# Kernel optimization log

Hardware: AMD Instinct MI355X
Metric: run time of the kernel (lower is better)

## Reference

```python
import jax, jax.numpy as jnp
import numpy as np

B, S, D = 4, 2048, 1024
H = 16
HD = D // H  # 64


def _xavier(key, shape):
    fan_in, fan_out = shape[1], shape[0]
    limit = float(np.sqrt(6.0 / (fan_in + fan_out)))
    return jax.random.uniform(key, shape, jnp.float32, -limit, limit)


def setup_inputs() -> dict:
    key = jax.random.key(0)
    ks = jax.random.split(key, 5)
    x = jax.random.normal(ks[0], (B, S, D), dtype=jnp.float32)
    # nn.Linear weights are [out, in]; biases zero-initialized
    Wq = _xavier(ks[1], (D, D)); bq = jnp.zeros((D,), jnp.float32)
    Wk = _xavier(ks[2], (D, D)); bk = jnp.zeros((D,), jnp.float32)
    Wv = _xavier(ks[3], (D, D)); bv = jnp.zeros((D,), jnp.float32)
    Wo = _xavier(ks[4], (D, D)); bo = jnp.zeros((D,), jnp.float32)
    return {"x": x, "Wq": Wq, "bq": bq, "Wk": Wk, "bk": bk,
            "Wv": Wv, "bv": bv, "Wo": Wo, "bo": bo}


def reference(x, Wq, bq, Wk, bk, Wv, bv, Wo, bo):
    # Projections (torch Linear: y = x @ W.T + b), reshape to [B, H, S, HD]
    def proj(W, b):
        y = jnp.einsum('bsd,ed->bse', x, W) + b
        return y.reshape(B, S, H, HD).transpose(0, 2, 1, 3)

    q = proj(Wq, bq)
    k = proj(Wk, bk)
    v = proj(Wv, bv)

    scale = 1.0 / jnp.sqrt(jnp.float32(HD))
    scores = jnp.einsum('bhqd,bhkd->bhqk', q, k) * scale  # [B,H,S,S]
    probs = jax.nn.softmax(scores, axis=-1)
    ctx = jnp.einsum('bhqk,bhkd->bhqd', probs, v)  # [B,H,S,HD]
    ctx = ctx.transpose(0, 2, 1, 3).reshape(B, S, D)
    out = jnp.einsum('bsd,ed->bse', ctx, Wo) + bo
    return out
```

## Files before the change

kernel.cpp:

```cpp
#include <hip/hip_runtime.h>
#include <hip/hip_bf16.h>
#include <stdint.h>


typedef __bf16 bf16;
typedef __bf16 bf16x8 __attribute__((ext_vector_type(8)));
typedef __bf16 bf16x4 __attribute__((ext_vector_type(4)));
typedef float  f32x4  __attribute__((ext_vector_type(4)));

#define MFMA_BF16(A, B, C) __builtin_amdgcn_mfma_f32_16x16x32_bf16(A, B, C, 0, 0, 0)
#define EXP2F(x) __builtin_amdgcn_exp2f(x)

#define ASYNC_CP16(DST_LDS, SRC_G)                                            \
  __builtin_amdgcn_global_load_lds(                                           \
      (__attribute__((address_space(1))) void*)(SRC_G),                       \
      (__attribute__((address_space(3))) void*)(DST_LDS), 16, 0, 0)

__global__ __launch_bounds__(256) void cvt5(
    const float* __restrict__ s0, bf16* __restrict__ d0, int n0,
    const float* __restrict__ s1, bf16* __restrict__ d1, int n1,
    const float* __restrict__ s2, bf16* __restrict__ d2, int n2,
    const float* __restrict__ s3, bf16* __restrict__ d3, int n3,
    const float* __restrict__ s4, bf16* __restrict__ d4, int n4)
{
  const float* s; bf16* d; int n;
  switch (blockIdx.y) {
    case 0: s = s0; d = d0; n = n0; break;
    case 1: s = s1; d = d1; n = n1; break;
    case 2: s = s2; d = d2; n = n2; break;
    case 3: s = s3; d = d3; n = n3; break;
    default: s = s4; d = d4; n = n4; break;
  }
  const int stride = gridDim.x * blockDim.x * 4;
  for (int i = (blockIdx.x * blockDim.x + threadIdx.x) * 4; i < n; i += stride) {
    const float4 v = *(const float4*)(s + i);
    bf16x4 o;
    o[0] = (bf16)v.x; o[1] = (bf16)v.y; o[2] = (bf16)v.z; o[3] = (bf16)v.w;
    *(bf16x4*)(d + i) = o;
  }
}

__global__ __launch_bounds__(256, 4) void gemm_qkv(
    const bf16* __restrict__ X,
    const bf16* __restrict__ Wq, const bf16* __restrict__ Wk,
    const bf16* __restrict__ Wv,
    const float* __restrict__ bq, const float* __restrict__ bk,
    const float* __restrict__ bv,
    bf16* __restrict__ Qo, bf16* __restrict__ Ko, bf16* __restrict__ Vo,
    float qscale)
{
  constexpr int N = 1024, K = 1024;
  __shared__ alignas(16) bf16 As[8192];
  __shared__ alignas(16) bf16 Bs[8192];

  const int sel = blockIdx.x >> 3;
  const bf16*  W    = (sel == 0) ? Wq : (sel == 1) ? Wk : Wv;
  const float* bias = (sel == 0) ? bq : (sel == 1) ? bk : bv;
  bf16*        Y    = (sel == 0) ? Qo : (sel == 1) ? Ko : Vo;
  const float scale = (sel == 0) ? qscale : 1.0f;

  const int tid  = threadIdx.x;
  const int lane = tid & 63;
  const int wv   = tid >> 6;
  const int l15  = lane & 15;
  const int quad = lane >> 4;
  const int wm   = (wv >> 1) * 64;
  const int wn   = (wv & 1) * 64;
  const int nbase = (blockIdx.x & 7) * 128;
  const int mbase = blockIdx.y * 128;

  f32x4 acc[4][4];
  #pragma unroll
  for (int i = 0; i < 4; ++i)
    #pragma unroll
    for (int j = 0; j < 4; ++j)
      acc[i][j] = (f32x4){0.f, 0.f, 0.f, 0.f};

  const int r8 = lane >> 3;
  const int oc = (lane & 7) ^ r8;
  const size_t lrowA = (size_t)(mbase + wv * 32 + r8);
  const size_t lrowB = (size_t)(nbase + wv * 32 + r8);

  for (int kb = 0; kb < K; kb += 64) {
    #pragma unroll
    for (int c = 0; c < 4; ++c) {
      ASYNC_CP16(As + (wv * 32 + c * 8) * 64, X + (lrowA + c * 8) * K + kb + oc * 8);
      ASYNC_CP16(Bs + (wv * 32 + c * 8) * 64, W + (lrowB + c * 8) * K + kb + oc * 8);
    }
    __syncthreads();
    #pragma unroll
    for (int ks = 0; ks < 2; ++ks) {
      bf16x8 af[4], bfr[4];
      #pragma unroll
      for (int t = 0; t < 4; ++t) {
        const int ma = wm + t * 16 + l15;
        af[t]  = *(const bf16x8*)(As + (ma * 8 + ((ks * 4 + quad) ^ (ma & 7))) * 8);
        const int nb = wn + t * 16 + l15;
        bfr[t] = *(const bf16x8*)(Bs + (nb * 8 + ((ks * 4 + quad) ^ (nb & 7))) * 8);
      }
      #pragma unroll
      for (int i = 0; i < 4; ++i)
        #pragma unroll
        for (int j = 0; j < 4; ++j)
          acc[i][j] = MFMA_BF16(af[i], bfr[j], acc[i][j]);
    }
    __syncthreads();
  }

  #pragma unroll
  for (int i = 0; i < 4; ++i) {
    const int row0 = mbase + wm + i * 16 + quad * 4;
    #pragma unroll
    for (int j = 0; j < 4; ++j) {
      const int col = nbase + wn + j * 16 + l15;
      const float bv2 = bias[col];
      #pragma unroll
      for (int r = 0; r < 4; ++r) {
        const float v = (acc[i][j][r] + bv2) * scale;
        const int row = row0 + r;
        if (sel != 2) {
          Y[(size_t)row * N + col] = (bf16)v;
        } else {
          const int bb = row >> 11, s  = row & 2047;
          const int hh = col >> 6,  hd = col & 63;
          Y[(size_t)(bb * 16 + hh) * (2048 * 64) + (size_t)(s >> 6) * 4096 +
            hd * 64 + (s & 63)] = (bf16)v;
        }
      }
    }
  }
}

__global__ __launch_bounds__(256) void gemm_o(
    const bf16* __restrict__ X, const bf16* __restrict__ W,
    const float* __restrict__ bias, float* __restrict__ Yf)
{
  constexpr int N = 1024, K = 1024;
  __shared__ alignas(16) bf16 As[8192];
  __shared__ alignas(16) bf16 Bs[8192];

  const int tid  = threadIdx.x;
  const int lane = tid & 63;
  const int wv   = tid >> 6;
  const int l15  = lane & 15;
  const int quad = lane >> 4;
  const int wm   = (wv >> 1) * 64;
  const int wn   = (wv & 1) * 64;
  const int nbase = blockIdx.x * 128;
  const int mbase = blockIdx.y * 128;

  f32x4 acc[4][4];
  #pragma unroll
  for (int i = 0; i < 4; ++i)
    #pragma unroll
    for (int j = 0; j < 4; ++j)
      acc[i][j] = (f32x4){0.f, 0.f, 0.f, 0.f};

  const int r8 = lane >> 3;
  const int oc = (lane & 7) ^ r8;
  const size_t lrowA = (size_t)(mbase + wv * 32 + r8);
  const size_t lrowB = (size_t)(nbase + wv * 32 + r8);

  for (int kb = 0; kb < K; kb += 64) {
    #pragma unroll
    for (int c = 0; c < 4; ++c) {
      ASYNC_CP16(As + (wv * 32 + c * 8) * 64, X + (lrowA + c * 8) * K + kb + oc * 8);
      ASYNC_CP16(Bs + (wv * 32 + c * 8) * 64, W + (lrowB + c * 8) * K + kb + oc * 8);
    }
    __syncthreads();
    #pragma unroll
    for (int ks = 0; ks < 2; ++ks) {
      bf16x8 af[4], bfr[4];
      #pragma unroll
      for (int t = 0; t < 4; ++t) {
        const int ma = wm + t * 16 + l15;
        af[t]  = *(const bf16x8*)(As + (ma * 8 + ((ks * 4 + quad) ^ (ma & 7))) * 8);
        const int nb = wn + t * 16 + l15;
        bfr[t] = *(const bf16x8*)(Bs + (nb * 8 + ((ks * 4 + quad) ^ (nb & 7))) * 8);
      }
      #pragma unroll
      for (int i = 0; i < 4; ++i)
        #pragma unroll
        for (int j = 0; j < 4; ++j)
          acc[i][j] = MFMA_BF16(af[i], bfr[j], acc[i][j]);
    }
    __syncthreads();
  }

  #pragma unroll
  for (int i = 0; i < 4; ++i) {
    const int row0 = mbase + wm + i * 16 + quad * 4;
    #pragma unroll
    for (int j = 0; j < 4; ++j) {
      const int col = nbase + wn + j * 16 + l15;
      const float bv2 = bias[col];
      #pragma unroll
      for (int r = 0; r < 4; ++r)
        Yf[(size_t)(row0 + r) * N + col] = acc[i][j][r] + bv2;
    }
  }
}

__global__ __launch_bounds__(256, 4) void attn(
    const bf16* __restrict__ Qb, const bf16* __restrict__ Kb,
    const bf16* __restrict__ Vt, bf16* __restrict__ Ob)
{
  constexpr int S = 2048, D = 1024;
  __shared__ alignas(16) bf16 Ks[2][4096];
  __shared__ alignas(16) bf16 Vs[2][4096];

  const int tid  = threadIdx.x;
  const int lane = tid & 63;
  const int wv   = tid >> 6;
  const int l15  = lane & 15;
  const int q0   = lane >> 4;

  const int L   = blockIdx.x;
  const int xcd = L & 7;
  const int ix  = L >> 3;
  const int bh  = xcd * 8 + (ix >> 4);
  const int qb  = ix & 15;
  const int b = bh >> 4, h = bh & 15;
  const int qblk = qb * 128 + wv * 32;

  bf16x8 qf[2][2];
  #pragma unroll
  for (int qt = 0; qt < 2; ++qt)
    #pragma unroll
    for (int dh = 0; dh < 2; ++dh)
      qf[qt][dh] = *(const bf16x8*)(
          Qb + (size_t)(b * S + qblk + qt * 16 + l15) * D + h * 64 + dh * 32 + q0 * 8);

  bf16x8 ones;
  #pragma unroll
  for (int i = 0; i < 8; ++i) ones[i] = (bf16)1.0f;

  f32x4 lacc[2];
  lacc[0] = (f32x4){0.f, 0.f, 0.f, 0.f};
  lacc[1] = (f32x4){0.f, 0.f, 0.f, 0.f};

  f32x4 o[4][2];
  #pragma unroll
  for (int ht = 0; ht < 4; ++ht)
    #pragma unroll
    for (int qt = 0; qt < 2; ++qt)
      o[ht][qt] = (f32x4){0.f, 0.f, 0.f, 0.f};

  const int r8a = lane >> 3;
  const int oc1 = (lane & 7) ^ (r8a & 3);
  const int oc2 = oc1 ^ 4;
  const int ov  = (lane & 7) ^ r8a;
  const bf16* kgw = Kb + (size_t)(b * S) * D + h * 64 + (size_t)(16 * wv) * D;
  const bf16* vgw = Vt + (size_t)(b * 16 + h) * (2048 * 64) + (16 * wv) * 64;

#define STAGE(KC, BUF)                                                        \
  {                                                                           \
    const bf16* ks = kgw + (size_t)(KC) * D;                                  \
    ASYNC_CP16(&Ks[BUF][wv * 1024],       ks + (size_t)r8a * D + oc1 * 8);    \
    ASYNC_CP16(&Ks[BUF][wv * 1024 + 512], ks + (size_t)(8 + r8a) * D + oc2 * 8);\
    const bf16* vs = vgw + (KC) * 64;                                         \
    ASYNC_CP16(&Vs[BUF][wv * 1024],       vs + r8a * 64 + ov * 8);            \
    ASYNC_CP16(&Vs[BUF][wv * 1024 + 512], vs + (8 + r8a) * 64 + ov * 8);      \
  }

  const int kla = 8 * (l15 >> 2) + (l15 & 3);
  const int swa = (l15 & 3) | (((l15 >> 2) & 1) << 2);
  const int swv = l15 & 7;

  STAGE(0, 0);

  for (int kc = 0, it = 0; kc < S; kc += 64, ++it) {
    const int cur = it & 1;
    __syncthreads();
    if (kc + 64 < S) STAGE(kc + 64, cur ^ 1);

    __builtin_amdgcn_s_setprio(1);

    f32x4 sc[2][4];
    #pragma unroll
    for (int kt = 0; kt < 4; ++kt) {
      const int key = kla + 4 * (kt & 1) + 32 * (kt >> 1);
      const bf16x8 kf0 = *(const bf16x8*)(&Ks[cur][(key * 8 + (q0 ^ swa)) * 8]);
      const bf16x8 kf1 = *(const bf16x8*)(&Ks[cur][(key * 8 + ((q0 + 4) ^ swa)) * 8]);
      #pragma unroll
      for (int qt = 0; qt < 2; ++qt) {
        f32x4 s = MFMA_BF16(kf0, qf[qt][0], ((f32x4){0.f, 0.f, 0.f, 0.f}));
        sc[qt][kt] = MFMA_BF16(kf1, qf[qt][1], s);
      }
    }

    bf16x8 pb[2][2];
    #pragma unroll
    for (int qt = 0; qt < 2; ++qt) {
      #pragma unroll
      for (int kt = 0; kt < 4; ++kt)
        #pragma unroll
        for (int r = 0; r < 4; ++r)
          pb[qt][kt >> 1][(kt & 1) * 4 + r] = (bf16)EXP2F(sc[qt][kt][r]);
    }

    #pragma unroll
    for (int qt = 0; qt < 2; ++qt) {
      lacc[qt] = MFMA_BF16(ones, pb[qt][0], lacc[qt]);
      lacc[qt] = MFMA_BF16(ones, pb[qt][1], lacc[qt]);
    }

    #pragma unroll
    for (int ht = 0; ht < 4; ++ht) {
      const int row = ht * 16 + l15;
      const bf16x8 vf0 = *(const bf16x8*)(&Vs[cur][(row * 8 + (q0 ^ swv)) * 8]);
      const bf16x8 vf1 = *(const bf16x8*)(&Vs[cur][(row * 8 + ((q0 + 4) ^ swv)) * 8]);
      #pragma unroll
      for (int qt = 0; qt < 2; ++qt) {
        o[ht][qt] = MFMA_BF16(vf0, pb[qt][0], o[ht][qt]);
        o[ht][qt] = MFMA_BF16(vf1, pb[qt][1], o[ht][qt]);
      }
    }

    __builtin_amdgcn_s_setprio(0);
  }
#undef STAGE

  #pragma unroll
  for (int qt = 0; qt < 2; ++qt) {
    const float inv = 1.0f / lacc[qt][0];
    bf16* orow = Ob + (size_t)(b * S + qblk + qt * 16 + l15) * D + h * 64 + q0 * 4;
    #pragma unroll
    for (int ht = 0; ht < 4; ++ht) {
      bf16x4 w;
      w[0] = (bf16)(o[ht][qt][0] * inv);
      w[1] = (bf16)(o[ht][qt][1] * inv);
      w[2] = (bf16)(o[ht][qt][2] * inv);
      w[3] = (bf16)(o[ht][qt][3] * inv);
      *(bf16x4*)(orow + ht * 16) = w;
    }
  }
}

extern "C" void kernel_launch(void* const* d_in, const int* in_sizes, int n_in,
                              void* d_out, int out_size, void* d_ws, size_t ws_size,
                              hipStream_t stream)
{
  const float* x  = (const float*)d_in[0];
  const float* Wq = (const float*)d_in[1];
  const float* bq = (const float*)d_in[2];
  const float* Wk = (const float*)d_in[3];
  const float* bk = (const float*)d_in[4];
  const float* Wv = (const float*)d_in[5];
  const float* bv = (const float*)d_in[6];
  const float* Wo = (const float*)d_in[7];
  const float* bo = (const float*)d_in[8];
  float* out = (float*)d_out;

  const size_t NX = (size_t)8192 * 1024;
  const size_t NW = (size_t)1024 * 1024;

  bf16* xb  = (bf16*)d_ws;
  bf16* Wqb = xb  + NX;
  bf16* Wkb = Wqb + NW;
  bf16* Wvb = Wkb + NW;
  bf16* Wob = Wvb + NW;
  bf16* Qb  = Wob + NW;
  bf16* Kb  = Qb  + NX;
  bf16* Vt  = Kb  + NX;
  bf16* Ctx = Vt  + NX;

  const float QSCALE = 0.18033688011112042f;

  dim3 bc(256, 1, 1);
  hipLaunchKernelGGL(cvt5, dim3(1024, 5, 1), bc, 0, stream,
                     x, xb, (int)NX, Wq, Wqb, (int)NW, Wk, Wkb, (int)NW,
                     Wv, Wvb, (int)NW, Wo, Wob, (int)NW);

  hipLaunchKernelGGL(gemm_qkv, dim3(24, 64, 1), bc, 0, stream,
                     xb, Wqb, Wkb, Wvb, bq, bk, bv, Qb, Kb, Vt, QSCALE);

  hipLaunchKernelGGL(attn, dim3(1024, 1, 1), bc, 0, stream, Qb, Kb, Vt, Ctx);

  hipLaunchKernelGGL(gemm_o, dim3(8, 64, 1), bc, 0, stream, Ctx, Wob, bo, out);
}
```

Before: 280.5 us.

## Double-buffer LDS tiles in projection GEMMs with BK=32 prefetch

Both projection GEMMs now stage K-tiles of 32 into two LDS buffers. The next tile is prefetched asynchronously while MFMAs run on the current one, and the per-iteration barrier count drops from two to one. The swizzle is reworked for 32-wide rows. The total LDS footprint is unchanged, but each iteration does half as much work per sync. Correctness relies on the async copy completing before the next barrier.

```diff
diff --git a/kernel.cpp b/kernel.cpp
--- a/kernel.cpp
+++ b/kernel.cpp
@@ -50,8 +50,8 @@
     float qscale)
 {
   constexpr int N = 1024, K = 1024;
-  __shared__ alignas(16) bf16 As[8192];
-  __shared__ alignas(16) bf16 Bs[8192];
+  __shared__ alignas(16) bf16 As[2][4096];
+  __shared__ alignas(16) bf16 Bs[2][4096];
 
   const int sel = blockIdx.x >> 3;
   const bf16*  W    = (sel == 0) ? Wq : (sel == 1) ? Wk : Wv;
@@ -76,36 +76,44 @@
     for (int j = 0; j < 4; ++j)
       acc[i][j] = (f32x4){0.f, 0.f, 0.f, 0.f};
 
-  const int r8 = lane >> 3;
-  const int oc = (lane & 7) ^ r8;
-  const size_t lrowA = (size_t)(mbase + wv * 32 + r8);
-  const size_t lrowB = (size_t)(nbase + wv * 32 + r8);
-
-  for (int kb = 0; kb < K; kb += 64) {
-    #pragma unroll
-    for (int c = 0; c < 4; ++c) {
-      ASYNC_CP16(As + (wv * 32 + c * 8) * 64, X + (lrowA + c * 8) * K + kb + oc * 8);
-      ASYNC_CP16(Bs + (wv * 32 + c * 8) * 64, W + (lrowB + c * 8) * K + kb + oc * 8);
-    }
+  const int rA  = lane >> 2;
+  const int ocn = (lane & 3) ^ ((rA >> 1) & 3);
+  const size_t lrowA = (size_t)(mbase + wv * 32 + rA);
+  const size_t lrowB = (size_t)(nbase + wv * 32 + rA);
+
+#define GSTAGE(BUF, KB)                                                       \
+  {                                                                           \
+    _Pragma("unroll")                                                         \
+    for (int c = 0; c < 2; ++c) {                                             \
+      ASYNC_CP16(&As[BUF][(wv * 32 + c * 16) * 32],                           \
+                 X + (lrowA + c * 16) * K + (KB) + ocn * 8);                  \
+      ASYNC_CP16(&Bs[BUF][(wv * 32 + c * 16) * 32],                           \
+                 W + (lrowB + c * 16) * K + (KB) + ocn * 8);                  \
+    }                                                                         \
+  }
+
+  GSTAGE(0, 0);
+  const int sw = (l15 >> 1) & 3;
+  int cur = 0;
+  for (int kb = 0; kb < K; kb += 32) {
     __syncthreads();
-    #pragma unroll
-    for (int ks = 0; ks < 2; ++ks) {
-      bf16x8 af[4], bfr[4];
-      #pragma unroll
-      for (int t = 0; t < 4; ++t) {
-        const int ma = wm + t * 16 + l15;
-        af[t]  = *(const bf16x8*)(As + (ma * 8 + ((ks * 4 + quad) ^ (ma & 7))) * 8);
-        const int nb = wn + t * 16 + l15;
-        bfr[t] = *(const bf16x8*)(Bs + (nb * 8 + ((ks * 4 + quad) ^ (nb & 7))) * 8);
-      }
-      #pragma unroll
-      for (int i = 0; i < 4; ++i)
-        #pragma unroll
-        for (int j = 0; j < 4; ++j)
-          acc[i][j] = MFMA_BF16(af[i], bfr[j], acc[i][j]);
-    }
-    __syncthreads();
-  }
+    if (kb + 32 < K) GSTAGE(cur ^ 1, kb + 32);
+    bf16x8 af[4], bfr[4];
+    #pragma unroll
+    for (int t = 0; t < 4; ++t) {
+      const int ma = wm + t * 16 + l15;
+      af[t]  = *(const bf16x8*)(&As[cur][ma * 32 + (quad ^ sw) * 8]);
+      const int nb = wn + t * 16 + l15;
+      bfr[t] = *(const bf16x8*)(&Bs[cur][nb * 32 + (quad ^ sw) * 8]);
+    }
+    #pragma unroll
+    for (int i = 0; i < 4; ++i)
+      #pragma unroll
+      for (int j = 0; j < 4; ++j)
+        acc[i][j] = MFMA_BF16(af[i], bfr[j], acc[i][j]);
+    cur ^= 1;
+  }
+#undef GSTAGE
 
   #pragma unroll
   for (int i = 0; i < 4; ++i) {
@@ -136,8 +144,8 @@
     const float* __restrict__ bias, float* __restrict__ Yf)
 {
   constexpr int N = 1024, K = 1024;
-  __shared__ alignas(16) bf16 As[8192];
-  __shared__ alignas(16) bf16 Bs[8192];
+  __shared__ alignas(16) bf16 As[2][4096];
+  __shared__ alignas(16) bf16 Bs[2][4096];
 
   const int tid  = threadIdx.x;
   const int lane = tid & 63;
@@ -156,36 +164,44 @@
     for (int j = 0; j < 4; ++j)
       acc[i][j] = (f32x4){0.f, 0.f, 0.f, 0.f};
 
-  const int r8 = lane >> 3;
-  const int oc = (lane & 7) ^ r8;
-  const size_t lrowA = (size_t)(mbase + wv * 32 + r8);
-  const size_t lrowB = (size_t)(nbase + wv * 32 + r8);
-
-  for (int kb = 0; kb < K; kb += 64) {
-    #pragma unroll
-    for (int c = 0; c < 4; ++c) {
-      ASYNC_CP16(As + (wv * 32 + c * 8) * 64, X + (lrowA + c * 8) * K + kb + oc * 8);
-      ASYNC_CP16(Bs + (wv * 32 + c * 8) * 64, W + (lrowB + c * 8) * K + kb + oc * 8);
-    }
+  const int rA  = lane >> 2;
+  const int ocn = (lane & 3) ^ ((rA >> 1) & 3);
+  const size_t lrowA = (size_t)(mbase + wv * 32 + rA);
+  const size_t lrowB = (size_t)(nbase + wv * 32 + rA);
+
+#define GSTAGE(BUF, KB)                                                       \
+  {                                                                           \
+    _Pragma("unroll")                                                         \
+    for (int c = 0; c < 2; ++c) {                                             \
+      ASYNC_CP16(&As[BUF][(wv * 32 + c * 16) * 32],                           \
+                 X + (lrowA + c * 16) * K + (KB) + ocn * 8);                  \
+      ASYNC_CP16(&Bs[BUF][(wv * 32 + c * 16) * 32],                           \
+                 W + (lrowB + c * 16) * K + (KB) + ocn * 8);                  \
+    }                                                                         \
+  }
+
+  GSTAGE(0, 0);
+  const int sw = (l15 >> 1) & 3;
+  int cur = 0;
+  for (int kb = 0; kb < K; kb += 32) {
     __syncthreads();
-    #pragma unroll
-    for (int ks = 0; ks < 2; ++ks) {
-      bf16x8 af[4], bfr[4];
-      #pragma unroll
-      for (int t = 0; t < 4; ++t) {
-        const int ma = wm + t * 16 + l15;
-        af[t]  = *(const bf16x8*)(As + (ma * 8 + ((ks * 4 + quad) ^ (ma & 7))) * 8);
-        const int nb = wn + t * 16 + l15;
-        bfr[t] = *(const bf16x8*)(Bs + (nb * 8 + ((ks * 4 + quad) ^ (nb & 7))) * 8);
-      }
-      #pragma unroll
-      for (int i = 0; i < 4; ++i)
-        #pragma unroll
-        for (int j = 0; j < 4; ++j)
-          acc[i][j] = MFMA_BF16(af[i], bfr[j], acc[i][j]);
-    }
-    __syncthreads();
-  }
+    if (kb + 32 < K) GSTAGE(cur ^ 1, kb + 32);
+    bf16x8 af[4], bfr[4];
+    #pragma unroll
+    for (int t = 0; t < 4; ++t) {
+      const int ma = wm + t * 16 + l15;
+      af[t]  = *(const bf16x8*)(&As[cur][ma * 32 + (quad ^ sw) * 8]);
+      const int nb = wn + t * 16 + l15;
+      bfr[t] = *(const bf16x8*)(&Bs[cur][nb * 32 + (quad ^ sw) * 8]);
+    }
+    #pragma unroll
+    for (int i = 0; i < 4; ++i)
+      #pragma unroll
+      for (int j = 0; j < 4; ++j)
+        acc[i][j] = MFMA_BF16(af[i], bfr[j], acc[i][j]);
+    cur ^= 1;
+  }
+#undef GSTAGE
 
   #pragma unroll
   for (int i = 0; i < 4; ++i) {
```

Result: slower. 295.8 us (+5.5%).
